# Kernel optimization log

Hardware: AMD Instinct MI355X
Metric: run time of the kernel (lower is better)

## Reference

```python
import jax, jax.numpy as jnp
import numpy as np

L = 16          # hash-grid levels (opt.L)
F = 2           # features per level
N_MIN = 16      # base resolution
T = 1 << 19     # hashmap size per level (log2_T = 19, bound == 1)
BOUND = 1.0
B = float(np.exp(np.log(512.0 / 16.0) / (L - 1)))  # per-level scale
PRIMES = np.array([1, 2654435761, 805459861], dtype=np.uint32)
# 8 corner offsets of the trilinear cell, in {0,1}^3
OFFS = np.array([[i, j, k] for i in (0, 1) for j in (0, 1) for k in (0, 1)], dtype=np.float32)


def hash_grid_encode(xn, tables):
    """xn: [N,3] in [0,1]; tables: [L,T,F]. Returns [N, L*F]."""
    offs_f = jnp.asarray(OFFS)                      # [8,3] float
    offs_u = jnp.asarray(OFFS.astype(np.uint32))    # [8,3] uint32
    primes = jnp.asarray(PRIMES)
    feats = []
    for l in range(L):
        res = int(np.floor(N_MIN * B ** l))
        pos = xn * res                              # [N,3]
        pf = jnp.minimum(jnp.floor(pos), float(res - 1))
        frac = pos - pf                             # [N,3], grads flow to x
        base = pf.astype(jnp.uint32)                # [N,3]
        corners = base[:, None, :] + offs_u[None]   # [N,8,3]
        if (res + 1) ** 3 <= T:
            # grid fits in table: coherent dense indexing (tcnn behavior)
            stride = jnp.asarray(np.array([1, res + 1, (res + 1) ** 2], dtype=np.uint32))
            idx = (corners * stride).sum(-1)        # [N,8]
        else:
            h = corners * primes                    # uint32 wraps (mod 2^32)
            idx = (h[..., 0] ^ h[..., 1] ^ h[..., 2]) & jnp.uint32(T - 1)
        vals = tables[l, idx.astype(jnp.int32)]     # [N,8,F] gather
        w = jnp.prod(jnp.where(offs_f[None] > 0, frac[:, None, :], 1.0 - frac[:, None, :]), axis=-1)  # [N,8]
        feats.append(jnp.einsum('nc,ncf->nf', w, vals))
    return jnp.concatenate(feats, axis=-1)          # [N, L*F]


def _wn(v, g):
    # torch weight_norm, dim=0: per-output-row normalization
    return g[:, None] * v / jnp.linalg.norm(v, axis=1, keepdims=True)


def setup_inputs() -> dict:
    key = jax.random.key(0)
    k = jax.random.split(key, 4)
    N = 2097152
    x = jax.random.uniform(k[0], (N, 3), jnp.float32, -BOUND, BOUND)
    tables = jax.random.normal(k[1], (L, T, F), jnp.float32) * 1e-2
    v1 = jax.random.normal(k[2], (64, L * F), jnp.float32) * (1.0 / np.sqrt(L * F))
    g1 = jnp.ones((64,), jnp.float32)
    b1 = jnp.zeros((64,), jnp.float32)
    v2 = jax.random.normal(k[3], (3, 64), jnp.float32) * (1.0 / 8.0)
    g2 = jnp.ones((3,), jnp.float32)
    b2 = jnp.zeros((3,), jnp.float32)
    return {"x": x, "tables": tables, "v1": v1, "g1": g1, "b1": b1,
            "v2": v2, "g2": g2, "b2": b2}


def reference(x, tables, v1, g1, b1, v2, g2, b2):
    xn = (x + BOUND) / (2.0 * BOUND)                # map to [0,1]
    h = hash_grid_encode(xn, tables)                # [N, 32]
    h1 = jax.nn.relu(h @ _wn(v1, g1).T + b1)        # [N, 64]
    out = jnp.tanh(h1 @ _wn(v2, g2).T + b2)         # [N, 3]
    return out
```

## Files before the change

kernel.cpp:

```cpp
#include <hip/hip_runtime.h>
#include <math.h>

#define LVL 16
#define TBL (1u << 19)
#define PR1 2654435761u
#define PR2 805459861u
#define NDENSE 7
#define NHASH 9
#define NXY 5

typedef __attribute__((ext_vector_type(4))) float f4;
typedef __attribute__((ext_vector_type(4))) unsigned u4;
typedef __attribute__((ext_vector_type(8))) short bf16x8;
typedef __attribute__((ext_vector_type(4))) float f32x4;

union FragU { unsigned u[4]; bf16x8 v; };

struct EncParams {
    float resf[LVL];
    float resm1[LVL];
    unsigned s1[LVL];
    unsigned s2[LVL];
    unsigned dense_mask;
};

struct FinalParams {
    float resf[NDENSE];
    float resm1[NDENSE];
    unsigned s1[NDENSE];
    unsigned s2[NDENSE];
    unsigned cellbase[NXY];
    unsigned cres[NXY];
    unsigned cres2[NXY];
    unsigned off1_5, off1_6;
};

struct CellBuild {
    unsigned nc[NXY];
    unsigned res[NXY];
    unsigned s1[NXY], s2[NXY];
    unsigned dst_dw[NXY];
};

static __device__ __forceinline__ unsigned f2bf(float f) {
    unsigned u = __float_as_uint(f);
    u += 0x7FFFu + ((u >> 16) & 1u);
    return u >> 16;
}
static __device__ __forceinline__ float bf_lo(unsigned p) { return __uint_as_float(p << 16); }
static __device__ __forceinline__ float bf_hi(unsigned p) { return __uint_as_float(p & 0xFFFF0000u); }

static __device__ __forceinline__ float fast_tanh(float v) {
    v = fminf(fmaxf(v, -10.f), 10.f);
    float e = __expf(2.0f * v);
    return __fdividef(e - 1.0f, e + 1.0f);
}

static __device__ __forceinline__ void gather8_sc0(const unsigned* __restrict__ tb,
                                                   const unsigned* off, unsigned* val)
{
    asm volatile(
        "global_load_dword %0, %8, %16 sc0\n\t"
        "global_load_dword %1, %9, %16 sc0\n\t"
        "global_load_dword %2, %10, %16 sc0\n\t"
        "global_load_dword %3, %11, %16 sc0\n\t"
        "global_load_dword %4, %12, %16 sc0\n\t"
        "global_load_dword %5, %13, %16 sc0\n\t"
        "global_load_dword %6, %14, %16 sc0\n\t"
        "global_load_dword %7, %15, %16 sc0\n\t"
        "s_waitcnt vmcnt(0)"
        : "=&v"(val[0]), "=&v"(val[1]), "=&v"(val[2]), "=&v"(val[3]),
          "=&v"(val[4]), "=&v"(val[5]), "=&v"(val[6]), "=&v"(val[7])
        : "v"(off[0]), "v"(off[1]), "v"(off[2]), "v"(off[3]),
          "v"(off[4]), "v"(off[5]), "v"(off[6]), "v"(off[7]),
          "s"(tb)
        : "memory");
}

static __device__ __forceinline__ void gather4x2_sc0(const unsigned* __restrict__ tb,
                                                     const unsigned* off,
                                                     unsigned long long* val)
{
    asm volatile(
        "global_load_dwordx2 %0, %4, %8 sc0\n\t"
        "global_load_dwordx2 %1, %5, %8 sc0\n\t"
        "global_load_dwordx2 %2, %6, %8 sc0\n\t"
        "global_load_dwordx2 %3, %7, %8 sc0\n\t"
        "s_waitcnt vmcnt(0)"
        : "=&v"(val[0]), "=&v"(val[1]), "=&v"(val[2]), "=&v"(val[3])
        : "v"(off[0]), "v"(off[1]), "v"(off[2]), "v"(off[3]),
          "s"(tb)
        : "memory");
}

static __device__ __forceinline__ void gather8x2_sc0(const unsigned* __restrict__ tb,
                                                     const unsigned* off,
                                                     unsigned long long* val)
{
    asm volatile(
        "global_load_dwordx2 %0, %8, %16 sc0\n\t"
        "global_load_dwordx2 %1, %9, %16 sc0\n\t"
        "global_load_dwordx2 %2, %10, %16 sc0\n\t"
        "global_load_dwordx2 %3, %11, %16 sc0\n\t"
        "global_load_dwordx2 %4, %12, %16 sc0\n\t"
        "global_load_dwordx2 %5, %13, %16 sc0\n\t"
        "global_load_dwordx2 %6, %14, %16 sc0\n\t"
        "global_load_dwordx2 %7, %15, %16 sc0\n\t"
        "s_waitcnt vmcnt(0)"
        : "=&v"(val[0]), "=&v"(val[1]), "=&v"(val[2]), "=&v"(val[3]),
          "=&v"(val[4]), "=&v"(val[5]), "=&v"(val[6]), "=&v"(val[7])
        : "v"(off[0]), "v"(off[1]), "v"(off[2]), "v"(off[3]),
          "v"(off[4]), "v"(off[5]), "v"(off[6]), "v"(off[7]),
          "s"(tb)
        : "memory");
}

static __device__ __forceinline__ void gather10x4_sc0(const unsigned* __restrict__ tb,
                                                      const unsigned* off, u4* val)
{
    asm volatile(
        "global_load_dwordx4 %0, %10, %20 sc0\n\t"
        "global_load_dwordx4 %1, %11, %20 sc0\n\t"
        "global_load_dwordx4 %2, %12, %20 sc0\n\t"
        "global_load_dwordx4 %3, %13, %20 sc0\n\t"
        "global_load_dwordx4 %4, %14, %20 sc0\n\t"
        "global_load_dwordx4 %5, %15, %20 sc0\n\t"
        "global_load_dwordx4 %6, %16, %20 sc0\n\t"
        "global_load_dwordx4 %7, %17, %20 sc0\n\t"
        "global_load_dwordx4 %8, %18, %20 sc0\n\t"
        "global_load_dwordx4 %9, %19, %20 sc0\n\t"
        "s_waitcnt vmcnt(0)"
        : "=&v"(val[0]), "=&v"(val[1]), "=&v"(val[2]), "=&v"(val[3]), "=&v"(val[4]),
          "=&v"(val[5]), "=&v"(val[6]), "=&v"(val[7]), "=&v"(val[8]), "=&v"(val[9])
        : "v"(off[0]), "v"(off[1]), "v"(off[2]), "v"(off[3]), "v"(off[4]),
          "v"(off[5]), "v"(off[6]), "v"(off[7]), "v"(off[8]), "v"(off[9]),
          "s"(tb)
        : "memory");
}

__global__ __launch_bounds__(256)
void prep_weights(const float* __restrict__ v1, const float* __restrict__ g1,
                  const float* __restrict__ v2, const float* __restrict__ g2,
                  float* __restrict__ ws)
{
    int t = threadIdx.x;
    if (t < 64) {
        float row[32];
        float s = 0.f;
        for (int i = 0; i < 32; ++i) { row[i] = v1[t * 32 + i]; s += row[i] * row[i]; }
        float sc = g1[t] / sqrtf(s);
        unsigned* wbf = (unsigned*)ws + 2304;
        for (int i = 0; i < 32; ++i) ws[t * 32 + i] = row[i] * sc;
        for (int w = 0; w < 16; ++w)
            wbf[t * 16 + w] = (f2bf(row[2 * w + 1] * sc) << 16) | f2bf(row[2 * w] * sc);
    } else if (t < 67) {
        int r = t - 64;
        float s = 0.f;
        for (int i = 0; i < 64; ++i) { float v = v2[r * 64 + i]; s += v * v; }
        float scale = g2[r] / sqrtf(s);
        for (int i = 0; i < 64; ++i) ws[2048 + r * 64 + i] = v2[r * 64 + i] * scale;
    }
}

__global__ __launch_bounds__(256)
void convert_tables(const float* __restrict__ src, unsigned* __restrict__ dst, int npairs)
{
    int j = blockIdx.x * 256 + threadIdx.x;
    if (j >= npairs) return;
    f4 v = __builtin_nontemporal_load((const f4*)src + j);
    unsigned lo = (f2bf(v.y) << 16) | f2bf(v.x);
    unsigned hi = (f2bf(v.w) << 16) | f2bf(v.z);
    unsigned long long o = ((unsigned long long)hi << 32) | lo;
    __builtin_nontemporal_store(o, (unsigned long long*)dst + j);
}

__global__ __launch_bounds__(256)
void build_cell(const float* __restrict__ tables, unsigned* __restrict__ region, CellBuild cb)
{
    int l = blockIdx.y;
    unsigned c = blockIdx.x * 256 + threadIdx.x;
    if (c >= cb.nc[l]) return;
    unsigned res = cb.res[l];
    unsigned cx = c % res, t = c / res;
    unsigned cy = t % res, cz = t / res;
    unsigned s1 = cb.s1[l], s2 = cb.s2[l];
    unsigned base = cx + cy * s1 + cz * s2;
    const float* src = tables + (size_t)l * TBL * 2;
    unsigned o[8];
#pragma unroll
    for (int k = 0; k < 8; ++k) {
        unsigned e = base + (k & 1u) + ((k >> 1) & 1u) * s1 + (k >> 2) * s2;
        o[k] = (f2bf(src[2 * e + 1]) << 16) | f2bf(src[2 * e]);
    }
    u4* dst = (u4*)(region + cb.dst_dw[l] + 8u * c);
    u4 o0 = {o[0], o[1], o[2], o[3]};
    u4 o1 = {o[4], o[5], o[6], o[7]};
    dst[0] = o0; dst[1] = o1;
}

__global__ __launch_bounds__(256)
void build_pair1(unsigned* __restrict__ region, unsigned src_dw, unsigned dst_dw, unsigned n)
{
    unsigned e = blockIdx.x * 256 + threadIdx.x;
    if (e + 1 < n)
        region[dst_dw + e] = region[src_dw + e + 1];
}

__global__ __launch_bounds__(256, 4)
void encode_hash4(const float* __restrict__ x, const unsigned* __restrict__ tb,
                  unsigned* __restrict__ hout, int N, float rf, float rm1)
{
    int j = blockIdx.x * 256 + threadIdx.x;
    int i0 = 4 * j;
    if (i0 >= N) return;

    if (i0 + 4 <= N) {
        const f4* xp = (const f4*)(x + (size_t)3 * i0);
        f4 q0 = __builtin_nontemporal_load(xp);
        f4 q1 = __builtin_nontemporal_load(xp + 1);
        f4 q2 = __builtin_nontemporal_load(xp + 2);
        float n0[4], n1[4], n2[4];
        n0[0] = (q0.x + 1.f) * 0.5f; n1[0] = (q0.y + 1.f) * 0.5f; n2[0] = (q0.z + 1.f) * 0.5f;
        n0[1] = (q0.w + 1.f) * 0.5f; n1[1] = (q1.x + 1.f) * 0.5f; n2[1] = (q1.y + 1.f) * 0.5f;
        n0[2] = (q1.z + 1.f) * 0.5f; n1[2] = (q1.w + 1.f) * 0.5f; n2[2] = (q2.x + 1.f) * 0.5f;
        n0[3] = (q2.y + 1.f) * 0.5f; n1[3] = (q2.z + 1.f) * 0.5f; n2[3] = (q2.w + 1.f) * 0.5f;

        unsigned o[4];
#pragma unroll
        for (int p = 0; p < 4; ++p) {
            float a0 = n0[p] * rf, a1 = n1[p] * rf, a2 = n2[p] * rf;
            float w0 = fminf(floorf(a0), rm1);
            float w1 = fminf(floorf(a1), rm1);
            float w2 = fminf(floorf(a2), rm1);
            float f0 = a0 - w0, f1 = a1 - w1, f2 = a2 - w2;
            unsigned c0 = (unsigned)w0;
            unsigned hx0 = c0, hx1 = c0 + 1u;
            unsigned hy0 = (unsigned)w1 * PR1, hy1 = hy0 + PR1;
            unsigned hz0 = (unsigned)w2 * PR2, hz1 = hz0 + PR2;

            float acc0, acc1;
            if (!(c0 & 1u)) {
                unsigned pb[4], qq[4];
#pragma unroll
                for (int jj = 0; jj < 4; ++jj) {
                    unsigned hyv = (jj & 2) ? hy1 : hy0;
                    unsigned hzv = (jj & 1) ? hz1 : hz0;
                    unsigned idx0 = (hx0 ^ hyv ^ hzv) & (TBL - 1u);
                    qq[jj] = idx0 & 1u;
                    pb[jj] = (idx0 & ~1u) << 2;
                }
                unsigned long long pv[4];
                gather4x2_sc0(tb, pb, pv);
                float wx1 = f0, wx0 = 1.f - f0;
                acc0 = 0.f; acc1 = 0.f;
#pragma unroll
                for (int jj = 0; jj < 4; ++jj) {
                    unsigned lo = (unsigned)pv[jj];
                    unsigned hi = (unsigned)(pv[jj] >> 32);
                    unsigned x0 = qq[jj] ? hi : lo;
                    unsigned x1 = qq[jj] ? lo : hi;
                    float wyz = ((jj & 2) ? f1 : 1.f - f1) * ((jj & 1) ? f2 : 1.f - f2);
                    acc0 = fmaf(wyz, fmaf(wx0, bf_lo(x0), wx1 * bf_lo(x1)), acc0);
                    acc1 = fmaf(wyz, fmaf(wx0, bf_hi(x0), wx1 * bf_hi(x1)), acc1);
                }
            } else {
                unsigned off[8];
#pragma unroll
                for (int c = 0; c < 8; ++c) {
                    unsigned hx = (c & 4) ? hx1 : hx0;
                    unsigned hy = (c & 2) ? hy1 : hy0;
                    unsigned hz = (c & 1) ? hz1 : hz0;
                    off[c] = ((hx ^ hy ^ hz) & (TBL - 1u)) << 2;
                }
                unsigned v[8];
                gather8_sc0(tb, off, v);
                acc0 = 0.f; acc1 = 0.f;
#pragma unroll
                for (int c = 0; c < 8; ++c) {
                    float w = ((c & 4) ? f0 : 1.f - f0) *
                              ((c & 2) ? f1 : 1.f - f1) *
                              ((c & 1) ? f2 : 1.f - f2);
                    acc0 = fmaf(w, bf_lo(v[c]), acc0);
                    acc1 = fmaf(w, bf_hi(v[c]), acc1);
                }
            }
            o[p] = (f2bf(acc1) << 16) | f2bf(acc0);
        }
        u4 ov = {o[0], o[1], o[2], o[3]};
        __builtin_nontemporal_store(ov, (u4*)(hout + i0));
    } else {
        for (int i = i0; i < N; ++i) {
            float xn0 = (x[3 * i + 0] + 1.0f) * 0.5f;
            float xn1 = (x[3 * i + 1] + 1.0f) * 0.5f;
            float xn2 = (x[3 * i + 2] + 1.0f) * 0.5f;
            float p0 = xn0 * rf, p1 = xn1 * rf, p2 = xn2 * rf;
            float pf0 = fminf(floorf(p0), rm1), pf1 = fminf(floorf(p1), rm1), pf2 = fminf(floorf(p2), rm1);
            float fg0 = p0 - pf0, fg1 = p1 - pf1, fg2 = p2 - pf2;
            unsigned hx0 = (unsigned)pf0, hx1 = hx0 + 1u;
            unsigned hy0 = (unsigned)pf1 * PR1, hy1 = hy0 + PR1;
            unsigned hz0 = (unsigned)pf2 * PR2, hz1 = hz0 + PR2;
            float a0 = 0.f, a1 = 0.f;
#pragma unroll
            for (int c = 0; c < 8; ++c) {
                unsigned hxv = (c & 4) ? hx1 : hx0;
                unsigned hyv = (c & 2) ? hy1 : hy0;
                unsigned hzv = (c & 1) ? hz1 : hz0;
                unsigned vv = tb[(hxv ^ hyv ^ hzv) & (TBL - 1u)];
                float w = ((c & 4) ? fg0 : 1.f - fg0) * ((c & 2) ? fg1 : 1.f - fg1) * ((c & 1) ? fg2 : 1.f - fg2);
                a0 = fmaf(w, bf_lo(vv), a0);
                a1 = fmaf(w, bf_hi(vv), a1);
            }
            hout[i] = (f2bf(a1) << 16) | f2bf(a0);
        }
    }
}

__global__ __launch_bounds__(256, 4)
void final_mfma(const float* __restrict__ x, const unsigned* __restrict__ tb,
                const unsigned* __restrict__ hbuf, const unsigned* __restrict__ w1bf,
                const float* __restrict__ b1, const float* __restrict__ w2,
                const float* __restrict__ b2, float* __restrict__ out,
                int N, FinalParams dp)
{
    __shared__ unsigned lds[256 * 20];
    int tid = threadIdx.x;
    int i = blockIdx.x * 256 + tid;

    unsigned hp[NHASH];
#pragma unroll
    for (int l = 0; l < NHASH; ++l)
        hp[l] = __builtin_nontemporal_load(hbuf + (size_t)l * N + i);

    float xn0 = (__builtin_nontemporal_load(x + 3 * i + 0) + 1.0f) * 0.5f;
    float xn1 = (__builtin_nontemporal_load(x + 3 * i + 1) + 1.0f) * 0.5f;
    float xn2 = (__builtin_nontemporal_load(x + 3 * i + 2) + 1.0f) * 0.5f;

    float fr[NDENSE][3];
    unsigned cc[NDENSE][3];
#pragma unroll
    for (int l = 0; l < NDENSE; ++l) {
        float rf = dp.resf[l];
        float p0 = xn0 * rf, p1 = xn1 * rf, p2 = xn2 * rf;
        float pf0 = fminf(floorf(p0), dp.resm1[l]);
        float pf1 = fminf(floorf(p1), dp.resm1[l]);
        float pf2 = fminf(floorf(p2), dp.resm1[l]);
        fr[l][0] = p0 - pf0; fr[l][1] = p1 - pf1; fr[l][2] = p2 - pf2;
        cc[l][0] = (unsigned)pf0; cc[l][1] = (unsigned)pf1; cc[l][2] = (unsigned)pf2;
    }

    unsigned offxy[2 * NXY];
#pragma unroll
    for (int l = 0; l < NXY; ++l) {
        unsigned c = cc[l][0] + cc[l][1] * dp.cres[l] + cc[l][2] * dp.cres2[l];
        unsigned base = dp.cellbase[l] + c * 32u;
        offxy[2 * l + 0] = base;
        offxy[2 * l + 1] = base + 16u;
    }
    unsigned off56[8];
#pragma unroll
    for (int h = 0; h < 2; ++h) {
        int l = 5 + h;
        unsigned base0 = l * (TBL * 4u);
        unsigned base1 = h ? dp.off1_6 : dp.off1_5;
        unsigned s1 = dp.s1[l], s2 = dp.s2[l];
        unsigned b = cc[l][0] + cc[l][1] * s1 + cc[l][2] * s2;
#pragma unroll
        for (int jj = 0; jj < 4; ++jj) {
            unsigned e = b + ((jj & 2) ? s1 : 0u) + ((jj & 1) ? s2 : 0u);
            off56[4 * h + jj] = (e & 1u) ? (base1 + ((e - 1u) << 2)) : (base0 + (e << 2));
        }
    }

    unsigned hw[16];
    {
        u4 xv[2 * NXY];
        gather10x4_sc0(tb, offxy, xv);
#pragma unroll
        for (int l = 0; l < NXY; ++l) {
            float wx1 = fr[l][0], wx0 = 1.f - wx1;
            float wy1 = fr[l][1], wy0 = 1.f - wy1;
            float wz1 = fr[l][2];
            float acc0 = 0.f, acc1 = 0.f;
#pragma unroll
            for (int z = 0; z < 2; ++z) {
                u4 e = xv[2 * l + z];
                float wz = z ? wz1 : 1.f - wz1;
                float lo = wy0 * fmaf(wx0, bf_lo(e[0]), wx1 * bf_lo(e[1]))
                         + wy1 * fmaf(wx0, bf_lo(e[2]), wx1 * bf_lo(e[3]));
                float hi = wy0 * fmaf(wx0, bf_hi(e[0]), wx1 * bf_hi(e[1]))
                         + wy1 * fmaf(wx0, bf_hi(e[2]), wx1 * bf_hi(e[3]));
                acc0 = fmaf(wz, lo, acc0);
                acc1 = fmaf(wz, hi, acc1);
            }
            hw[l] = (f2bf(acc1) << 16) | f2bf(acc0);
        }
    }
    {
        unsigned long long pv[8];
        gather8x2_sc0(tb, off56, pv);
#pragma unroll
        for (int h = 0; h < 2; ++h) {
            int l = 5 + h;
            float wx1 = fr[l][0], wx0 = 1.f - wx1;
            float f1v = fr[l][1], f2v = fr[l][2];
            float acc0 = 0.f, acc1 = 0.f;
#pragma unroll
            for (int jj = 0; jj < 4; ++jj) {
                unsigned long long pvv = pv[4 * h + jj];
                unsigned lo = (unsigned)pvv;
                unsigned hi = (unsigned)(pvv >> 32);
                float wyz = ((jj & 2) ? f1v : 1.f - f1v) * ((jj & 1) ? f2v : 1.f - f2v);
                acc0 = fmaf(wyz, fmaf(wx0, bf_lo(lo), wx1 * bf_lo(hi)), acc0);
                acc1 = fmaf(wyz, fmaf(wx0, bf_hi(lo), wx1 * bf_hi(hi)), acc1);
            }
            hw[l] = (f2bf(acc1) << 16) | f2bf(acc0);
        }
    }
#pragma unroll
    for (int l = 0; l < NHASH; ++l) hw[NDENSE + l] = hp[l];

    unsigned* row = &lds[tid * 20];
#pragma unroll
    for (int c = 0; c < 4; ++c)
        *(uint4*)(row + 4 * c) = make_uint4(hw[4 * c], hw[4 * c + 1], hw[4 * c + 2], hw[4 * c + 3]);

    __syncthreads();

    int lane = tid & 63;
    int wv   = tid >> 6;
    int l16  = lane & 15;
    int lhi  = lane >> 4;

    bf16x8 bfr[4];
#pragma unroll
    for (int t = 0; t < 4; ++t) {
        const unsigned* p = w1bf + (t * 16 + l16) * 16 + lhi * 4;
        FragU u;
        u.u[0] = p[0]; u.u[1] = p[1]; u.u[2] = p[2]; u.u[3] = p[3];
        bfr[t] = u.v;
    }
    float b1v[4];
#pragma unroll
    for (int t = 0; t < 4; ++t) b1v[t] = b1[t * 16 + l16];
    float w2v[3][4];
#pragma unroll
    for (int jj = 0; jj < 3; ++jj)
#pragma unroll
        for (int t = 0; t < 4; ++t) w2v[jj][t] = w2[jj * 64 + t * 16 + l16];
    float bias2 = (l16 < 3) ? b2[l16] : 0.f;

#pragma unroll
    for (int g = 0; g < 4; ++g) {
        const unsigned* rp = &lds[(wv * 64 + g * 16 + l16) * 20 + lhi * 4];
        FragU u;
        u.u[0] = rp[0]; u.u[1] = rp[1]; u.u[2] = rp[2]; u.u[3] = rp[3];
        bf16x8 af = u.v;

        f32x4 acc[4];
#pragma unroll
        for (int t = 0; t < 4; ++t) {
            f32x4 z = {0.f, 0.f, 0.f, 0.f};
            acc[t] = __builtin_amdgcn_mfma_f32_16x16x32_bf16(af, bfr[t], z, 0, 0, 0);
        }

#pragma unroll
        for (int r = 0; r < 4; ++r) {
            float p0 = 0.f, p1 = 0.f, p2 = 0.f;
#pragma unroll
            for (int t = 0; t < 4; ++t) {
                float a = fmaxf(acc[t][r] + b1v[t], 0.f);
                p0 = fmaf(a, w2v[0][t], p0);
                p1 = fmaf(a, w2v[1][t], p1);
                p2 = fmaf(a, w2v[2][t], p2);
            }
#pragma unroll
            for (int m = 1; m < 16; m <<= 1) {
                p0 += __shfl_xor(p0, m);
                p1 += __shfl_xor(p1, m);
                p2 += __shfl_xor(p2, m);
            }
            if (l16 < 3) {
                int point = blockIdx.x * 256 + wv * 64 + g * 16 + lhi * 4 + r;
                float v = (l16 == 0) ? p0 : ((l16 == 1) ? p1 : p2);
                out[(size_t)point * 3 + l16] = fast_tanh(v + bias2);
            }
        }
    }
}

__global__ __launch_bounds__(256)
void fused_ngp(const float* __restrict__ x, const float* __restrict__ tables,
               const float* __restrict__ w1, const float* __restrict__ b1,
               const float* __restrict__ w2, const float* __restrict__ b2,
               float* __restrict__ out, int N, EncParams ep)
{
    int i = blockIdx.x * 256 + threadIdx.x;
    if (i >= N) return;

    float xn0 = (x[3 * i + 0] + 1.0f) * 0.5f;
    float xn1 = (x[3 * i + 1] + 1.0f) * 0.5f;
    float xn2 = (x[3 * i + 2] + 1.0f) * 0.5f;

    float h[2 * LVL];

#pragma unroll
    for (int l = 0; l < LVL; ++l) {
        float rf = ep.resf[l];
        float p0 = xn0 * rf, p1 = xn1 * rf, p2 = xn2 * rf;
        float pf0 = fminf(floorf(p0), ep.resm1[l]);
        float pf1 = fminf(floorf(p1), ep.resm1[l]);
        float pf2 = fminf(floorf(p2), ep.resm1[l]);
        float fr0 = p0 - pf0, fr1 = p1 - pf1, fr2 = p2 - pf2;
        unsigned c0 = (unsigned)pf0, c1 = (unsigned)pf1, c2 = (unsigned)pf2;
        const float2* tb = (const float2*)tables + (size_t)l * TBL;

        float acc0 = 0.f, acc1 = 0.f;
        if ((ep.dense_mask >> l) & 1u) {
            unsigned s1 = ep.s1[l], s2 = ep.s2[l];
            unsigned b = c0 + c1 * s1 + c2 * s2;
#pragma unroll
            for (int c = 0; c < 8; ++c) {
                unsigned id = b + ((c & 4) ? 1u : 0u) + ((c & 2) ? s1 : 0u) + ((c & 1) ? s2 : 0u);
                float2 v = tb[id];
                float w = ((c & 4) ? fr0 : 1.f - fr0) * ((c & 2) ? fr1 : 1.f - fr1) * ((c & 1) ? fr2 : 1.f - fr2);
                acc0 = fmaf(w, v.x, acc0);
                acc1 = fmaf(w, v.y, acc1);
            }
        } else {
            unsigned hx0 = c0, hx1 = c0 + 1u;
            unsigned hy0 = c1 * PR1, hy1 = hy0 + PR1;
            unsigned hz0 = c2 * PR2, hz1 = hz0 + PR2;
#pragma unroll
            for (int c = 0; c < 8; ++c) {
                unsigned hx = (c & 4) ? hx1 : hx0;
                unsigned hy = (c & 2) ? hy1 : hy0;
                unsigned hz = (c & 1) ? hz1 : hz0;
                float2 v = tb[(hx ^ hy ^ hz) & (TBL - 1u)];
                float w = ((c & 4) ? fr0 : 1.f - fr0) * ((c & 2) ? fr1 : 1.f - fr1) * ((c & 1) ? fr2 : 1.f - fr2);
                acc0 = fmaf(w, v.x, acc0);
                acc1 = fmaf(w, v.y, acc1);
            }
        }
        h[2 * l + 0] = acc0;
        h[2 * l + 1] = acc1;
    }

    float r0 = b2[0], r1 = b2[1], r2 = b2[2];
    for (int o = 0; o < 64; ++o) {
        float a = b1[o];
#pragma unroll
        for (int k = 0; k < 32; ++k) a = fmaf(h[k], w1[o * 32 + k], a);
        a = fmaxf(a, 0.f);
        r0 = fmaf(a, w2[0 * 64 + o], r0);
        r1 = fmaf(a, w2[1 * 64 + o], r1);
        r2 = fmaf(a, w2[2 * 64 + o], r2);
    }
    out[3 * i + 0] = tanhf(r0);
    out[3 * i + 1] = tanhf(r1);
    out[3 * i + 2] = tanhf(r2);
}

extern "C" void kernel_launch(void* const* d_in, const int* in_sizes, int n_in,
                              void* d_out, int out_size, void* d_ws, size_t ws_size,
                              hipStream_t stream)
{
    const float* x      = (const float*)d_in[0];
    const float* tables = (const float*)d_in[1];
    const float* v1     = (const float*)d_in[2];
    const float* g1     = (const float*)d_in[3];
    const float* b1     = (const float*)d_in[4];
    const float* v2     = (const float*)d_in[5];
    const float* g2     = (const float*)d_in[6];
    const float* b2     = (const float*)d_in[7];
    float* out = (float*)d_out;
    float* ws  = (float*)d_ws;
    int N = in_sizes[0] / 3;

    EncParams ep;
    double Bd = exp(log(512.0 / 16.0) / (double)(LVL - 1));
    unsigned dm = 0;
    int resv[LVL];
    for (int l = 0; l < LVL; ++l) {
        int res = (int)floor(16.0 * pow(Bd, (double)l));
        resv[l] = res;
        ep.resf[l]  = (float)res;
        ep.resm1[l] = (float)(res - 1);
        long long rp1 = (long long)res + 1;
        if (rp1 * rp1 * rp1 <= (long long)TBL) dm |= (1u << l);
        ep.s1[l] = (unsigned)(res + 1);
        ep.s2[l] = (unsigned)((res + 1) * (res + 1));
    }
    ep.dense_mask = dm;

    prep_weights<<<1, 256, 0, stream>>>(v1, g1, v2, g2, ws);

    size_t tb_off_bytes = 16384;
    unsigned S[NDENSE], NC[NXY];
    for (int l = 0; l < NDENSE; ++l) {
        unsigned s1 = (unsigned)(resv[l] + 1);
        S[l] = s1 * s1 * s1;
    }
    for (int l = 0; l < NXY; ++l) {
        unsigned r = (unsigned)resv[l];
        NC[l] = r * r * r;
    }

    unsigned cum_dw = LVL * TBL;
    unsigned off1_5_dw = cum_dw; cum_dw += (S[5] + 3u) & ~1u;
    unsigned off1_6_dw = cum_dw; cum_dw += (S[6] + 3u) & ~1u;
    cum_dw = (cum_dw + 15u) & ~15u;
    unsigned cell_dw[NXY];
    unsigned maxNC = 0;
    for (int l = 0; l < NXY; ++l) {
        cell_dw[l] = cum_dw;
        cum_dw += 8u * NC[l];
        if (NC[l] > maxNC) maxNC = NC[l];
    }
    cum_dw = (cum_dw + 3u) & ~3u;
    size_t h_off_bytes = tb_off_bytes + (size_t)cum_dw * 4;
    size_t need = h_off_bytes + (size_t)NHASH * (size_t)N * 4;

    bool fast = (ws_size >= need) && (dm == 0x7Fu) && (N % 1024 == 0);
    if (fast) {
        unsigned* tb   = (unsigned*)((char*)d_ws + tb_off_bytes);
        unsigned* hbuf = (unsigned*)((char*)d_ws + h_off_bytes);
        unsigned* w1bf = (unsigned*)ws + 2304;

        int npairs = (int)((size_t)LVL * TBL / 2);
        convert_tables<<<(npairs + 255) / 256, 256, 0, stream>>>(tables, tb, npairs);

        CellBuild cb;
        for (int l = 0; l < NXY; ++l) {
            cb.nc[l] = NC[l]; cb.res[l] = (unsigned)resv[l];
            cb.s1[l] = ep.s1[l]; cb.s2[l] = ep.s2[l];
            cb.dst_dw[l] = cell_dw[l];
        }
        dim3 cgrid((maxNC + 255) / 256, NXY);
        build_cell<<<cgrid, 256, 0, stream>>>(tables, tb, cb);

        build_pair1<<<(S[5] + 255) / 256, 256, 0, stream>>>(tb, 5u * TBL, off1_5_dw, S[5]);
        build_pair1<<<(S[6] + 255) / 256, 256, 0, stream>>>(tb, 6u * TBL, off1_6_dw, S[6]);

        int grid4 = N / 1024;
        for (int l = 0; l < NHASH; ++l) {
            int gl = NDENSE + l;
            encode_hash4<<<grid4, 256, 0, stream>>>(
                x, tb + (size_t)gl * TBL, hbuf + (size_t)l * N, N,
                ep.resf[gl], ep.resm1[gl]);
        }

        FinalParams dp;
        for (int l = 0; l < NDENSE; ++l) {
            dp.resf[l] = ep.resf[l]; dp.resm1[l] = ep.resm1[l];
            dp.s1[l] = ep.s1[l];     dp.s2[l] = ep.s2[l];
        }
        for (int l = 0; l < NXY; ++l) {
            dp.cellbase[l] = cell_dw[l] * 4u;
            dp.cres[l] = (unsigned)resv[l];
            dp.cres2[l] = (unsigned)(resv[l] * resv[l]);
        }
        dp.off1_5 = off1_5_dw * 4u;
        dp.off1_6 = off1_6_dw * 4u;
        final_mfma<<<N / 256, 256, 0, stream>>>(x, tb, hbuf, w1bf, b1,
                                                ws + 2048, b2, out, N, dp);
    } else {
        fused_ngp<<<(N + 255) / 256, 256, 0, stream>>>(x, tables, ws, b1, ws + 2048, b2, out, N, ep);
    }
}
```

Before: 630.9 us.

## Use per-cell packed corner layout for all seven dense levels

Extends the per-cell layout, which stores all 8 corners of a cell contiguously in bf16, from the first five dense levels to all seven. Levels 0-4 now reuse the converted-table slots in place, and levels 5-6 get new cell regions. This replaces the pair-shifted dwordx2 gathers (eight per point) for levels 5 and 6 with four dwordx4 loads and removes the build_pair1 kernels. The cost is a larger build_cell pass and more memory for levels 5-6, and the shared blend helper leaves a dead fmaf path.

```diff
diff --git a/kernel.cpp b/kernel.cpp
--- a/kernel.cpp
+++ b/kernel.cpp
@@ -7,7 +7,6 @@
 #define PR2 805459861u
 #define NDENSE 7
 #define NHASH 9
-#define NXY 5
 
 typedef __attribute__((ext_vector_type(4))) float f4;
 typedef __attribute__((ext_vector_type(4))) unsigned u4;
@@ -27,19 +26,16 @@
 struct FinalParams {
     float resf[NDENSE];
     float resm1[NDENSE];
-    unsigned s1[NDENSE];
-    unsigned s2[NDENSE];
-    unsigned cellbase[NXY];
-    unsigned cres[NXY];
-    unsigned cres2[NXY];
-    unsigned off1_5, off1_6;
+    unsigned cellbase[NDENSE];
+    unsigned cres[NDENSE];
+    unsigned cres2[NDENSE];
 };
 
 struct CellBuild {
-    unsigned nc[NXY];
-    unsigned res[NXY];
-    unsigned s1[NXY], s2[NXY];
-    unsigned dst_dw[NXY];
+    unsigned nc[NDENSE];
+    unsigned res[NDENSE];
+    unsigned s1[NDENSE], s2[NDENSE];
+    unsigned dst_dw[NDENSE];
 };
 
 static __device__ __forceinline__ unsigned f2bf(float f) {
@@ -89,28 +85,6 @@
         "s_waitcnt vmcnt(0)"
         : "=&v"(val[0]), "=&v"(val[1]), "=&v"(val[2]), "=&v"(val[3])
         : "v"(off[0]), "v"(off[1]), "v"(off[2]), "v"(off[3]),
-          "s"(tb)
-        : "memory");
-}
-
-static __device__ __forceinline__ void gather8x2_sc0(const unsigned* __restrict__ tb,
-                                                     const unsigned* off,
-                                                     unsigned long long* val)
-{
-    asm volatile(
-        "global_load_dwordx2 %0, %8, %16 sc0\n\t"
-        "global_load_dwordx2 %1, %9, %16 sc0\n\t"
-        "global_load_dwordx2 %2, %10, %16 sc0\n\t"
-        "global_load_dwordx2 %3, %11, %16 sc0\n\t"
-        "global_load_dwordx2 %4, %12, %16 sc0\n\t"
-        "global_load_dwordx2 %5, %13, %16 sc0\n\t"
-        "global_load_dwordx2 %6, %14, %16 sc0\n\t"
-        "global_load_dwordx2 %7, %15, %16 sc0\n\t"
-        "s_waitcnt vmcnt(0)"
-        : "=&v"(val[0]), "=&v"(val[1]), "=&v"(val[2]), "=&v"(val[3]),
-          "=&v"(val[4]), "=&v"(val[5]), "=&v"(val[6]), "=&v"(val[7])
-        : "v"(off[0]), "v"(off[1]), "v"(off[2]), "v"(off[3]),
-          "v"(off[4]), "v"(off[5]), "v"(off[6]), "v"(off[7]),
           "s"(tb)
         : "memory");
 }
@@ -138,6 +112,21 @@
         : "memory");
 }
 
+static __device__ __forceinline__ void gather4x4_sc0(const unsigned* __restrict__ tb,
+                                                     const unsigned* off, u4* val)
+{
+    asm volatile(
+        "global_load_dwordx4 %0, %4, %8 sc0\n\t"
+        "global_load_dwordx4 %1, %5, %8 sc0\n\t"
+        "global_load_dwordx4 %2, %6, %8 sc0\n\t"
+        "global_load_dwordx4 %3, %7, %8 sc0\n\t"
+        "s_waitcnt vmcnt(0)"
+        : "=&v"(val[0]), "=&v"(val[1]), "=&v"(val[2]), "=&v"(val[3])
+        : "v"(off[0]), "v"(off[1]), "v"(off[2]), "v"(off[3]),
+          "s"(tb)
+        : "memory");
+}
+
 __global__ __launch_bounds__(256)
 void prep_weights(const float* __restrict__ v1, const float* __restrict__ g1,
                   const float* __restrict__ v2, const float* __restrict__ g2,
@@ -198,14 +187,6 @@
     dst[0] = o0; dst[1] = o1;
 }
 
-__global__ __launch_bounds__(256)
-void build_pair1(unsigned* __restrict__ region, unsigned src_dw, unsigned dst_dw, unsigned n)
-{
-    unsigned e = blockIdx.x * 256 + threadIdx.x;
-    if (e + 1 < n)
-        region[dst_dw + e] = region[src_dw + e + 1];
-}
-
 __global__ __launch_bounds__(256, 4)
 void encode_hash4(const float* __restrict__ x, const unsigned* __restrict__ tb,
                   unsigned* __restrict__ hout, int N, float rf, float rm1)
@@ -315,6 +296,26 @@
     }
 }
 
+static __device__ __forceinline__ unsigned blend_cell(u4 e0, u4 e1,
+                                                      float fx, float fy, float fz)
+{
+    float wx1 = fx, wx0 = 1.f - fx;
+    float wy1 = fy, wy0 = 1.f - fy;
+    float lo0 = wy0 * fmaf(wx0, bf_lo(e0[0]), wx1 * bf_lo(e0[1]))
+              + wy1 * fmaf(wx0, bf_lo(e0[2]), wx1 * bf_lo(e0[3]));
+    float hi0 = wy0 * fmaf(wx0, bf_hi(e0[0]), wx1 * bf_hi(e0[1]))
+              + wy1 * fmaf(wx0, bf_hi(e0[2]), wx1 * bf_hi(e0[3]));
+    float lo1 = wy0 * fmaf(wx0, bf_lo(e1[0]), wx1 * bf_lo(e1[1]))
+              + wy1 * fmaf(wx0, bf_lo(e1[2]), wx1 * bf_lo(e1[3]));
+    float hi1 = wy0 * fmaf(wx0, bf_hi(e1[0]), wx1 * bf_hi(e1[1]))
+              + wy1 * fmaf(wx0, bf_hi(e1[2]), wx1 * bf_hi(e1[3]));
+    float acc0 = fmaf(fz, lo1 - lo0, lo0);
+    float acc1 = fmaf(fz, hi1 - hi0, hi0);
+    acc0 = (1.f - fz) * lo0 + fz * lo1;
+    acc1 = (1.f - fz) * hi0 + fz * hi1;
+    return (f2bf(acc1) << 16) | f2bf(acc0);
+}
+
 __global__ __launch_bounds__(256, 4)
 void final_mfma(const float* __restrict__ x, const unsigned* __restrict__ tb,
                 const unsigned* __restrict__ hbuf, const unsigned* __restrict__ w1bf,
@@ -336,7 +337,7 @@
     float xn2 = (__builtin_nontemporal_load(x + 3 * i + 2) + 1.0f) * 0.5f;
 
     float fr[NDENSE][3];
-    unsigned cc[NDENSE][3];
+    unsigned offs[2 * NDENSE];
 #pragma unroll
     for (int l = 0; l < NDENSE; ++l) {
         float rf = dp.resf[l];
@@ -345,76 +346,25 @@
         float pf1 = fminf(floorf(p1), dp.resm1[l]);
         float pf2 = fminf(floorf(p2), dp.resm1[l]);
         fr[l][0] = p0 - pf0; fr[l][1] = p1 - pf1; fr[l][2] = p2 - pf2;
-        cc[l][0] = (unsigned)pf0; cc[l][1] = (unsigned)pf1; cc[l][2] = (unsigned)pf2;
-    }
-
-    unsigned offxy[2 * NXY];
-#pragma unroll
-    for (int l = 0; l < NXY; ++l) {
-        unsigned c = cc[l][0] + cc[l][1] * dp.cres[l] + cc[l][2] * dp.cres2[l];
+        unsigned c = (unsigned)pf0 + (unsigned)pf1 * dp.cres[l] + (unsigned)pf2 * dp.cres2[l];
         unsigned base = dp.cellbase[l] + c * 32u;
-        offxy[2 * l + 0] = base;
-        offxy[2 * l + 1] = base + 16u;
-    }
-    unsigned off56[8];
-#pragma unroll
-    for (int h = 0; h < 2; ++h) {
-        int l = 5 + h;
-        unsigned base0 = l * (TBL * 4u);
-        unsigned base1 = h ? dp.off1_6 : dp.off1_5;
-        unsigned s1 = dp.s1[l], s2 = dp.s2[l];
-        unsigned b = cc[l][0] + cc[l][1] * s1 + cc[l][2] * s2;
-#pragma unroll
-        for (int jj = 0; jj < 4; ++jj) {
-            unsigned e = b + ((jj & 2) ? s1 : 0u) + ((jj & 1) ? s2 : 0u);
-            off56[4 * h + jj] = (e & 1u) ? (base1 + ((e - 1u) << 2)) : (base0 + (e << 2));
-        }
+        offs[2 * l + 0] = base;
+        offs[2 * l + 1] = base + 16u;
     }
 
     unsigned hw[16];
     {
-        u4 xv[2 * NXY];
-        gather10x4_sc0(tb, offxy, xv);
-#pragma unroll
-        for (int l = 0; l < NXY; ++l) {
-            float wx1 = fr[l][0], wx0 = 1.f - wx1;
-            float wy1 = fr[l][1], wy0 = 1.f - wy1;
-            float wz1 = fr[l][2];
-            float acc0 = 0.f, acc1 = 0.f;
-#pragma unroll
-            for (int z = 0; z < 2; ++z) {
-                u4 e = xv[2 * l + z];
-                float wz = z ? wz1 : 1.f - wz1;
-                float lo = wy0 * fmaf(wx0, bf_lo(e[0]), wx1 * bf_lo(e[1]))
-                         + wy1 * fmaf(wx0, bf_lo(e[2]), wx1 * bf_lo(e[3]));
-                float hi = wy0 * fmaf(wx0, bf_hi(e[0]), wx1 * bf_hi(e[1]))
-                         + wy1 * fmaf(wx0, bf_hi(e[2]), wx1 * bf_hi(e[3]));
-                acc0 = fmaf(wz, lo, acc0);
-                acc1 = fmaf(wz, hi, acc1);
-            }
-            hw[l] = (f2bf(acc1) << 16) | f2bf(acc0);
-        }
+        u4 xv[10];
+        gather10x4_sc0(tb, offs, xv);
+#pragma unroll
+        for (int l = 0; l < 5; ++l)
+            hw[l] = blend_cell(xv[2 * l], xv[2 * l + 1], fr[l][0], fr[l][1], fr[l][2]);
     }
     {
-        unsigned long long pv[8];
-        gather8x2_sc0(tb, off56, pv);
-#pragma unroll
-        for (int h = 0; h < 2; ++h) {
-            int l = 5 + h;
-            float wx1 = fr[l][0], wx0 = 1.f - wx1;
-            float f1v = fr[l][1], f2v = fr[l][2];
-            float acc0 = 0.f, acc1 = 0.f;
-#pragma unroll
-            for (int jj = 0; jj < 4; ++jj) {
-                unsigned long long pvv = pv[4 * h + jj];
-                unsigned lo = (unsigned)pvv;
-                unsigned hi = (unsigned)(pvv >> 32);
-                float wyz = ((jj & 2) ? f1v : 1.f - f1v) * ((jj & 1) ? f2v : 1.f - f2v);
-                acc0 = fmaf(wyz, fmaf(wx0, bf_lo(lo), wx1 * bf_lo(hi)), acc0);
-                acc1 = fmaf(wyz, fmaf(wx0, bf_hi(lo), wx1 * bf_hi(hi)), acc1);
-            }
-            hw[l] = (f2bf(acc1) << 16) | f2bf(acc0);
-        }
+        u4 yv[4];
+        gather4x4_sc0(tb, offs + 10, yv);
+        hw[5] = blend_cell(yv[0], yv[1], fr[5][0], fr[5][1], fr[5][2]);
+        hw[6] = blend_cell(yv[2], yv[3], fr[6][0], fr[6][1], fr[6][2]);
     }
 #pragma unroll
     for (int l = 0; l < NHASH; ++l) hw[NDENSE + l] = hp[l];
@@ -595,32 +545,22 @@
     prep_weights<<<1, 256, 0, stream>>>(v1, g1, v2, g2, ws);
 
     size_t tb_off_bytes = 16384;
-    unsigned S[NDENSE], NC[NXY];
+    unsigned NC[NDENSE];
     for (int l = 0; l < NDENSE; ++l) {
-        unsigned s1 = (unsigned)(resv[l] + 1);
-        S[l] = s1 * s1 * s1;
-    }
-    for (int l = 0; l < NXY; ++l) {
         unsigned r = (unsigned)resv[l];
         NC[l] = r * r * r;
     }
+    bool cell_ok = true;
+    for (int l = 0; l < 5; ++l) if (8ull * NC[l] > TBL) cell_ok = false;
 
     unsigned cum_dw = LVL * TBL;
-    unsigned off1_5_dw = cum_dw; cum_dw += (S[5] + 3u) & ~1u;
-    unsigned off1_6_dw = cum_dw; cum_dw += (S[6] + 3u) & ~1u;
     cum_dw = (cum_dw + 15u) & ~15u;
-    unsigned cell_dw[NXY];
-    unsigned maxNC = 0;
-    for (int l = 0; l < NXY; ++l) {
-        cell_dw[l] = cum_dw;
-        cum_dw += 8u * NC[l];
-        if (NC[l] > maxNC) maxNC = NC[l];
-    }
-    cum_dw = (cum_dw + 3u) & ~3u;
+    unsigned cell5_dw = cum_dw; cum_dw += (8u * NC[5] + 15u) & ~15u;
+    unsigned cell6_dw = cum_dw; cum_dw += (8u * NC[6] + 15u) & ~15u;
     size_t h_off_bytes = tb_off_bytes + (size_t)cum_dw * 4;
     size_t need = h_off_bytes + (size_t)NHASH * (size_t)N * 4;
 
-    bool fast = (ws_size >= need) && (dm == 0x7Fu) && (N % 1024 == 0);
+    bool fast = (ws_size >= need) && (dm == 0x7Fu) && (N % 1024 == 0) && cell_ok;
     if (fast) {
         unsigned* tb   = (unsigned*)((char*)d_ws + tb_off_bytes);
         unsigned* hbuf = (unsigned*)((char*)d_ws + h_off_bytes);
@@ -630,16 +570,16 @@
         convert_tables<<<(npairs + 255) / 256, 256, 0, stream>>>(tables, tb, npairs);
 
         CellBuild cb;
-        for (int l = 0; l < NXY; ++l) {
+        unsigned maxNC = 0;
+        for (int l = 0; l < NDENSE; ++l) {
             cb.nc[l] = NC[l]; cb.res[l] = (unsigned)resv[l];
             cb.s1[l] = ep.s1[l]; cb.s2[l] = ep.s2[l];
-            cb.dst_dw[l] = cell_dw[l];
-        }
-        dim3 cgrid((maxNC + 255) / 256, NXY);
+            cb.dst_dw[l] = (l < 5) ? (unsigned)l * TBL
+                                   : ((l == 5) ? cell5_dw : cell6_dw);
+            if (NC[l] > maxNC) maxNC = NC[l];
+        }
+        dim3 cgrid((maxNC + 255) / 256, NDENSE);
         build_cell<<<cgrid, 256, 0, stream>>>(tables, tb, cb);
-
-        build_pair1<<<(S[5] + 255) / 256, 256, 0, stream>>>(tb, 5u * TBL, off1_5_dw, S[5]);
-        build_pair1<<<(S[6] + 255) / 256, 256, 0, stream>>>(tb, 6u * TBL, off1_6_dw, S[6]);
 
         int grid4 = N / 1024;
         for (int l = 0; l < NHASH; ++l) {
@@ -652,15 +592,11 @@
         FinalParams dp;
         for (int l = 0; l < NDENSE; ++l) {
             dp.resf[l] = ep.resf[l]; dp.resm1[l] = ep.resm1[l];
-            dp.s1[l] = ep.s1[l];     dp.s2[l] = ep.s2[l];
-        }
-        for (int l = 0; l < NXY; ++l) {
-            dp.cellbase[l] = cell_dw[l] * 4u;
+            dp.cellbase[l] = ((l < 5) ? (unsigned)l * TBL
+                                      : ((l == 5) ? cell5_dw : cell6_dw)) * 4u;
             dp.cres[l] = (unsigned)resv[l];
             dp.cres2[l] = (unsigned)(resv[l] * resv[l]);
         }
-        dp.off1_5 = off1_5_dw * 4u;
-        dp.off1_6 = off1_6_dw * 4u;
         final_mfma<<<N / 256, 256, 0, stream>>>(x, tb, hbuf, w1bf, b1,
                                                 ws + 2048, b2, out, N, dp);
     } else {
```

New measurement: 567.3 us. 10.1% less time.
